# Performance work log

Measured on AMD Instinct MI355X. Metric: run time of the kernel, lower is better.

## Reference

```python
import jax, jax.numpy as jnp
import numpy as np

B, C, N, H = 4, 512, 2048, 8
D = C // H  # per-head depth = 64
EPS = 1e-5


def conv1x1(x, W, b):
    # x: [B, Cin, N], W: [Cout, Cin], b: [Cout]
    return jnp.einsum('oc,bcn->bon', W, x) + b[None, :, None]


def instance_norm(x):
    # normalize over length dim per (batch, channel), no affine
    mu = jnp.mean(x, axis=-1, keepdims=True)
    var = jnp.var(x, axis=-1, keepdims=True)
    return (x - mu) * jax.lax.rsqrt(var + EPS)


def _pipeline(src, tgt, Wq, bq, Wk, bk, Wv, bv, Wm, bm):
    # query from src, key/value from tgt; reshape C -> (D outer, H inner)
    q = conv1x1(src, Wq, bq).reshape(B, D, H, N)
    k = conv1x1(tgt, Wk, bk).reshape(B, D, H, N)
    v = conv1x1(tgt, Wv, bv).reshape(B, D, H, N)
    scores = jnp.einsum('bdhn,bdhm->bhnm', q, k) / jnp.sqrt(jnp.float32(D))
    probs = jax.nn.softmax(scores, axis=-1)
    out = jnp.einsum('bhnm,bdhm->bdhn', probs, v).reshape(B, C, N)
    return conv1x1(out, Wm, bm)


def _mlp(x, W1, b1, W2, b2):
    h = conv1x1(x, W1, b1)
    h = jax.nn.relu(instance_norm(h))
    return conv1x1(h, W2, b2)


def setup_inputs() -> dict:
    key = jax.random.key(0)
    ks = jax.random.split(key, 8)
    s = 0.02
    return {
        'source_features': jax.random.normal(ks[0], (B, C, N), jnp.float32),
        'target_features': jax.random.normal(ks[1], (B, C, N), jnp.float32),
        'Wq': jax.random.normal(ks[2], (C, C), jnp.float32) * s,
        'bq': jnp.zeros((C,), jnp.float32),
        'Wk': jax.random.normal(ks[3], (C, C), jnp.float32) * s,
        'bk': jnp.zeros((C,), jnp.float32),
        'Wv': jax.random.normal(ks[4], (C, C), jnp.float32) * s,
        'bv': jnp.zeros((C,), jnp.float32),
        'Wm': jax.random.normal(ks[5], (C, C), jnp.float32) * s,
        'bm': jnp.zeros((C,), jnp.float32),
        'W1': jax.random.normal(ks[6], (2 * C, 2 * C), jnp.float32) * s,
        'b1': jnp.zeros((2 * C,), jnp.float32),
        'W2': jax.random.normal(ks[7], (C, 2 * C), jnp.float32) * s,
        'b2': jnp.zeros((C,), jnp.float32),
    }


def reference(source_features, target_features, Wq, bq, Wk, bk, Wv, bv, Wm, bm, W1, b1, W2, b2):
    src, tgt = source_features, target_features
    # source update uses ORIGINAL target features
    src_att = _pipeline(src, tgt, Wq, bq, Wk, bk, Wv, bv, Wm, bm)
    src = src + _mlp(jnp.concatenate([src, src_att], axis=1), W1, b1, W2, b2)
    # target update uses the UPDATED source features (in-place semantics of original)
    tgt_att = _pipeline(tgt, src, Wq, bq, Wk, bk, Wv, bv, Wm, bm)
    tgt = tgt + _mlp(jnp.concatenate([tgt, tgt_att], axis=1), W1, b1, W2, b2)
    return src, tgt
```

## Files before the change

### kernel.cpp

```cpp
#include <hip/hip_runtime.h>

#define NN 2048
#define CC 512
#define BB 4
#define HH 8
#define DD 64
#define SCALE 0.18033688011112043f

typedef unsigned short u16;
typedef __attribute__((ext_vector_type(8))) short bf16x8;
typedef __attribute__((ext_vector_type(4))) float f32x4;

extern "C" __device__ float __ocml_native_exp2_f32(float);

__device__ inline u16 f2b(float x) {
    unsigned u = __builtin_bit_cast(unsigned, x);
    u += 0x7fffu + ((u >> 16) & 1u);
    return (u16)(u >> 16);
}
__device__ inline float b2f(u16 h) {
    unsigned u = ((unsigned)h) << 16;
    return __builtin_bit_cast(float, u);
}

#define GLD16(g, l) __builtin_amdgcn_global_load_lds( \
    (const __attribute__((address_space(1))) unsigned int*)(g), \
    (__attribute__((address_space(3))) unsigned int*)(l), 16, 0, 0)

template<int JT>
__device__ __forceinline__ void gemm_core_t(
    const u16* __restrict__ Xa, const u16* __restrict__ Xb, int Ca, int K,
    const u16* __restrict__ Wt, size_t rowBase,
    u16* As, u16* Bs, f32x4 (&acc)[4][JT])
{
    constexpr int OT = JT * 32;
    const int tid = threadIdx.x;
    const int lane = tid & 63, w = tid >> 6;
    const int quad = lane >> 4, l16 = lane & 15;
    const int wrow = w & 1, wcol = w >> 1;
    const int arow = lane >> 2, aseg = lane & 3;

    for (int k0 = 0; k0 < K; k0 += 32) {
        const u16* Xs; int Crow, cc;
        if (k0 < Ca) { Xs = Xa; Crow = Ca; cc = k0; }
        else         { Xs = Xb; Crow = K - Ca; cc = k0 - Ca; }
#pragma unroll
        for (int i = 0; i < 2; ++i) {
            int rl = w * 32 + i * 16 + arow;
            int la = __builtin_amdgcn_readfirstlane((w * 32 + i * 16) * 32);
            GLD16(Xs + (rowBase + rl) * (size_t)Crow + cc + aseg * 8, (char*)As + (size_t)la * 2);
        }
#pragma unroll
        for (int i = 0; i < OT / 64; ++i) {
            int rl = w * (OT / 4) + i * 16 + arow;
            int la = __builtin_amdgcn_readfirstlane((w * (OT / 4) + i * 16) * 32);
            GLD16(Wt + (size_t)rl * K + k0 + aseg * 8, (char*)Bs + (size_t)la * 2);
        }
        __syncthreads();
        bf16x8 av[4], bv[JT];
#pragma unroll
        for (int i = 0; i < 4; ++i)
            av[i] = *(const bf16x8*)&As[(wrow * 64 + i * 16 + l16) * 32 + quad * 8];
#pragma unroll
        for (int jj = 0; jj < JT; ++jj)
            bv[jj] = *(const bf16x8*)&Bs[(wcol * JT * 16 + jj * 16 + l16) * 32 + quad * 8];
#pragma unroll
        for (int i = 0; i < 4; ++i)
#pragma unroll
            for (int jj = 0; jj < JT; ++jj)
                acc[i][jj] = __builtin_amdgcn_mfma_f32_16x16x32_bf16(av[i], bv[jj], acc[i][jj], 0, 0, 0);
        __syncthreads();
    }
}

template<int JT>
__device__ __forceinline__ void gemm_epilogue_t(
    f32x4 (&acc)[4][JT], const float* __restrict__ bias, int mode,
    int b, int n0, int o0, int Cout,
    const float* __restrict__ res, float* __restrict__ outF, u16* __restrict__ outB)
{
    const int tid = threadIdx.x;
    const int lane = tid & 63, w = tid >> 6;
    const int quad = lane >> 4, l16 = lane & 15;
    const int wrow = w & 1, wcol = w >> 1;
    const size_t bN = (size_t)b * NN;
    const int nb0 = n0 + wrow * 64, ob0 = o0 + wcol * JT * 16;

    if (mode == 0) {
#pragma unroll
        for (int j = 0; j < JT; ++j) {
            int o = ob0 + j * 16 + l16;
            float bs = bias[o];
#pragma unroll
            for (int i = 0; i < 4; ++i)
#pragma unroll
                for (int r = 0; r < 4; ++r) {
                    int n = nb0 + i * 16 + quad * 4 + r;
                    outB[(bN + n) * Cout + o] = f2b(acc[i][j][r] + bs);
                }
        }
    } else if (mode == 1) {
#pragma unroll
        for (int j = 0; j < JT; ++j) {
            int o = ob0 + j * 16 + l16;
            float bs = bias[o];
            int h = o >> 6, d = o & 63;
#pragma unroll
            for (int i = 0; i < 4; ++i) {
                int n = nb0 + i * 16 + quad * 4;
                ushort4 pk;
                pk.x = f2b(acc[i][j][0] + bs); pk.y = f2b(acc[i][j][1] + bs);
                pk.z = f2b(acc[i][j][2] + bs); pk.w = f2b(acc[i][j][3] + bs);
                *(ushort4*)&outB[(((size_t)b * HH + h) * DD + d) * NN + n] = pk;
            }
        }
    } else {
#pragma unroll
        for (int j = 0; j < JT; ++j) {
            int o = ob0 + j * 16 + l16;
            float bs = bias[o];
#pragma unroll
            for (int i = 0; i < 4; ++i) {
                int n = nb0 + i * 16 + quad * 4;
                size_t ad = ((size_t)b * Cout + o) * NN + n;
                float4 rv = *(const float4*)&res[ad];
                float4 yv;
                yv.x = acc[i][j][0] + bs + rv.x;
                yv.y = acc[i][j][1] + bs + rv.y;
                yv.z = acc[i][j][2] + bs + rv.z;
                yv.w = acc[i][j][3] + bs + rv.w;
                *(float4*)&outF[ad] = yv;
                if (mode == 2) {
                    outB[(bN + n + 0) * Cout + o] = f2b(yv.x);
                    outB[(bN + n + 1) * Cout + o] = f2b(yv.y);
                    outB[(bN + n + 2) * Cout + o] = f2b(yv.z);
                    outB[(bN + n + 3) * Cout + o] = f2b(yv.w);
                }
            }
        }
    }
}

template<int JT>
__global__ __launch_bounds__(256, (JT == 2 ? 4 : 3)) void gemm_bf16_t(
    const u16* __restrict__ Wb, const float* __restrict__ bias,
    const u16* __restrict__ Xa, const u16* __restrict__ Xb,
    int Ca, int K, int Cout,
    const float* __restrict__ res, float* __restrict__ outF,
    u16* __restrict__ outB, int mode)
{
    __shared__ u16 As[128 * 32];
    __shared__ u16 Bs[JT * 32 * 32];
    const int b = blockIdx.z, n0 = blockIdx.x * 128, o0 = blockIdx.y * (JT * 32);
    f32x4 acc[4][JT] = {};
    gemm_core_t<JT>(Xa, Xb, Ca, K, Wb + (size_t)o0 * K, (size_t)b * NN + n0, As, Bs, acc);
    gemm_epilogue_t<JT>(acc, bias, mode, b, n0, o0, Cout, res, outF, outB);
}

__global__ __launch_bounds__(256, 3) void gemm_qkv(
    const u16* __restrict__ WQ, const float* __restrict__ bQ,
    const u16* __restrict__ XQ, u16* __restrict__ outQ,
    const u16* __restrict__ WK, const float* __restrict__ bK, u16* __restrict__ outK,
    const u16* __restrict__ WV, const float* __restrict__ bV, u16* __restrict__ outV,
    const u16* __restrict__ XKV)
{
    __shared__ u16 As[128 * 32];
    __shared__ u16 Bs[128 * 32];
    const int yb = blockIdx.y;
    const u16* W; const float* bias; const u16* X; u16* outB; int mode, o0;
    if (yb < 4)      { o0 = yb * 128;       W = WQ; bias = bQ; X = XQ;  outB = outQ; mode = 0; }
    else if (yb < 8) { o0 = (yb - 4) * 128; W = WK; bias = bK; X = XKV; outB = outK; mode = 0; }
    else             { o0 = (yb - 8) * 128; W = WV; bias = bV; X = XKV; outB = outV; mode = 1; }
    const int b = blockIdx.z, n0 = blockIdx.x * 128;
    f32x4 acc[4][4] = {};
    gemm_core_t<4>(X, nullptr, 512, 512, W + (size_t)o0 * 512, (size_t)b * NN + n0, As, Bs, acc);
    gemm_epilogue_t<4>(acc, bias, mode, b, n0, o0, 512, nullptr, nullptr, outB);
}

__global__ __launch_bounds__(256, 2) void attn(
    const u16* __restrict__ Qg, const u16* __restrict__ Kg,
    const u16* __restrict__ Vg, u16* __restrict__ Og)
{
    __shared__ __align__(16) u16 Ks[2][64 * 64];
    __shared__ __align__(16) u16 Vt[2][64 * 64];
    __shared__ __align__(16) u16 Ps[128 * 64];
    const int tid = threadIdx.x;
    const int lane = tid & 63, w = tid >> 6;
    const int quad = lane >> 4, l16 = lane & 15;
    const int id = blockIdx.x;
    const int xcd = id & 7, jj = id >> 3;
    const int bh = xcd * 4 + (jj >> 4), nb = jj & 15;
    const int b = bh >> 3, h = bh & 7;
    const int n0 = nb * 128, wn0 = w * 32;
    const int sr0 = w * 16;
    const size_t qkBase = ((size_t)b * NN) * CC + h * DD;
    const size_t vBase  = (((size_t)b * HH + h) * DD) * NN;
    const int r8 = lane >> 3, seg = lane & 7;
    const int segp = seg ^ r8;
    const int lk = l16 & 7;

    const u16* kp0 = Kg + qkBase + (size_t)(sr0 + r8) * CC + segp * 8;
    const u16* kp1 = kp0 + (size_t)8 * CC;
    const u16* vp0 = Vg + vBase + (size_t)(sr0 + r8) * NN + segp * 8;
    const u16* vp1 = vp0 + (size_t)8 * NN;

    bf16x8 qf[2][2];
#pragma unroll
    for (int qs = 0; qs < 2; ++qs) {
        int n = n0 + wn0 + qs * 16 + l16;
#pragma unroll
        for (int ks = 0; ks < 2; ++ks)
            qf[qs][ks] = *(const bf16x8*)&Qg[qkBase + (size_t)n * CC + ks * 32 + quad * 8];
    }

    const short oneb = 0x3F80;
    const bf16x8 ones = {oneb, oneb, oneb, oneb, oneb, oneb, oneb, oneb};
    f32x4 oa[2][4] = {};
    f32x4 lacc[2] = {};

    GLD16(kp0, &Ks[0][sr0 * 64]);
    GLD16(kp1, &Ks[0][(sr0 + 8) * 64]);
    GLD16(vp0, &Vt[0][sr0 * 64]);
    GLD16(vp1, &Vt[0][(sr0 + 8) * 64]);
    kp0 += 64 * CC; kp1 += 64 * CC; vp0 += 64; vp1 += 64;

#define ATTN_PREF(BUF) do { \
        GLD16(kp0, &Ks[BUF][sr0 * 64]); \
        GLD16(kp1, &Ks[BUF][(sr0 + 8) * 64]); \
        GLD16(vp0, &Vt[BUF][sr0 * 64]); \
        GLD16(vp1, &Vt[BUF][(sr0 + 8) * 64]); \
        kp0 += 64 * CC; kp1 += 64 * CC; vp0 += 64; vp1 += 64; \
    } while (0)

#define ATTN_BODY(CUR) do { \
        const u16* ksb = Ks[CUR]; \
        const u16* vtb = Vt[CUR]; \
        f32x4 st[2][4] = {}; \
        _Pragma("unroll") \
        for (int ks = 0; ks < 2; ++ks) { \
            bf16x8 ak[4]; \
            _Pragma("unroll") \
            for (int rt = 0; rt < 4; ++rt) \
                ak[rt] = *(const bf16x8*)&ksb[(rt * 16 + l16) * 64 + ((ks * 4 + quad) ^ lk) * 8]; \
            __builtin_amdgcn_s_setprio(1); \
            _Pragma("unroll") \
            for (int rt = 0; rt < 4; ++rt) \
                _Pragma("unroll") \
                for (int qs = 0; qs < 2; ++qs) \
                    st[qs][rt] = __builtin_amdgcn_mfma_f32_16x16x32_bf16(ak[rt], qf[qs][ks], st[qs][rt], 0, 0, 0); \
            __builtin_amdgcn_s_setprio(0); \
        } \
        _Pragma("unroll") \
        for (int qs = 0; qs < 2; ++qs) { \
            int nrow = wn0 + qs * 16 + l16; \
            _Pragma("unroll") \
            for (int rt = 0; rt < 4; ++rt) { \
                unsigned u0 = __builtin_bit_cast(unsigned, __ocml_native_exp2_f32(st[qs][rt][0])); \
                unsigned u1 = __builtin_bit_cast(unsigned, __ocml_native_exp2_f32(st[qs][rt][1])); \
                unsigned u2 = __builtin_bit_cast(unsigned, __ocml_native_exp2_f32(st[qs][rt][2])); \
                unsigned u3 = __builtin_bit_cast(unsigned, __ocml_native_exp2_f32(st[qs][rt][3])); \
                uint2 t; \
                t.x = __builtin_amdgcn_perm(u1, u0, 0x07060302u); \
                t.y = __builtin_amdgcn_perm(u3, u2, 0x07060302u); \
                int g = (rt * 2 + (quad >> 1)) ^ lk; \
                *(uint2*)&Ps[nrow * 64 + g * 8 + (quad & 1) * 4] = t; \
            } \
        } \
        _Pragma("unroll") \
        for (int ks = 0; ks < 2; ++ks) { \
            bf16x8 pa[2]; \
            _Pragma("unroll") \
            for (int qs = 0; qs < 2; ++qs) \
                pa[qs] = *(const bf16x8*)&Ps[(wn0 + qs * 16 + l16) * 64 + ((ks * 4 + quad) ^ lk) * 8]; \
            bf16x8 vb[4]; \
            _Pragma("unroll") \
            for (int ct = 0; ct < 4; ++ct) \
                vb[ct] = *(const bf16x8*)&vtb[(ct * 16 + l16) * 64 + ((ks * 4 + quad) ^ lk) * 8]; \
            __builtin_amdgcn_s_setprio(1); \
            _Pragma("unroll") \
            for (int ct = 0; ct < 4; ++ct) \
                _Pragma("unroll") \
                for (int qs = 0; qs < 2; ++qs) \
                    oa[qs][ct] = __builtin_amdgcn_mfma_f32_16x16x32_bf16(pa[qs], vb[ct], oa[qs][ct], 0, 0, 0); \
            _Pragma("unroll") \
            for (int qs = 0; qs < 2; ++qs) \
                lacc[qs] = __builtin_amdgcn_mfma_f32_16x16x32_bf16(pa[qs], ones, lacc[qs], 0, 0, 0); \
            __builtin_amdgcn_s_setprio(0); \
        } \
    } while (0)

    for (int it = 0; it < NN / 64; it += 2) {
        __syncthreads();
        ATTN_PREF(1);
        ATTN_BODY(0);
        __syncthreads();
        if (it < NN / 64 - 2)
            ATTN_PREF(0);
        ATTN_BODY(1);
    }
#undef ATTN_PREF
#undef ATTN_BODY

#pragma unroll
    for (int qs = 0; qs < 2; ++qs)
#pragma unroll
        for (int r = 0; r < 4; ++r) {
            float li = 1.f / lacc[qs][r];
            int n = n0 + wn0 + qs * 16 + quad * 4 + r;
#pragma unroll
            for (int ct = 0; ct < 4; ++ct)
                Og[qkBase + (size_t)n * CC + ct * 16 + l16] = f2b(oa[qs][ct][r] * li);
        }
}

__global__ __launch_bounds__(256) void transpose_cvt(
    const float* __restrict__ X, u16* __restrict__ Y)
{
    __shared__ float T[64][65];
    const int tid = threadIdx.x;
    const int n0 = blockIdx.x * 64, c0 = blockIdx.y * 64, b = blockIdx.z;
    const int rr = tid >> 4, cc4 = tid & 15;
#pragma unroll
    for (int p = 0; p < 4; ++p) {
        int cl = p * 16 + rr;
        float4 v = *(const float4*)&X[((size_t)b * CC + c0 + cl) * NN + n0 + cc4 * 4];
        T[cl][cc4 * 4 + 0] = v.x; T[cl][cc4 * 4 + 1] = v.y;
        T[cl][cc4 * 4 + 2] = v.z; T[cl][cc4 * 4 + 3] = v.w;
    }
    __syncthreads();
#pragma unroll
    for (int p = 0; p < 4; ++p) {
        int nl = p * 16 + rr;
        ushort4 pk;
        pk.x = f2b(T[cc4 * 4 + 0][nl]);
        pk.y = f2b(T[cc4 * 4 + 1][nl]);
        pk.z = f2b(T[cc4 * 4 + 2][nl]);
        pk.w = f2b(T[cc4 * 4 + 3][nl]);
        *(ushort4*)&Y[((size_t)b * NN + n0 + nl) * CC + c0 + cc4 * 4] = pk;
    }
}

__global__ __launch_bounds__(256) void prep_weights(
    const float* __restrict__ Wq, const float* __restrict__ Wk,
    const float* __restrict__ Wv, const float* __restrict__ Wm,
    const float* __restrict__ W1, const float* __restrict__ W2,
    u16* oQ, u16* oK, u16* oV, u16* oM, u16* o1, u16* o2)
{
    const float* W; u16* o; int rows, cols, perm; float sc = 1.f;
    switch (blockIdx.z) {
        case 0: W = Wq; o = oQ; rows = 512;  cols = 512;  perm = 1; sc = SCALE; break;
        case 1: W = Wk; o = oK; rows = 512;  cols = 512;  perm = 1; break;
        case 2: W = Wv; o = oV; rows = 512;  cols = 512;  perm = 1; break;
        case 3: W = Wm; o = oM; rows = 512;  cols = 512;  perm = 2; break;
        case 4: W = W1; o = o1; rows = 1024; cols = 1024; perm = 0; break;
        default: W = W2; o = o2; rows = 512; cols = 1024; perm = 0; break;
    }
    int c = blockIdx.x * 256 + threadIdx.x;
    int r = blockIdx.y;
    if (r >= rows || c >= cols) return;
    int sr = r, scol = c;
    if (perm == 1) sr = (r & 63) * 8 + (r >> 6);
    else if (perm == 2) scol = (c & 63) * 8 + (c >> 6);
    o[(size_t)r * cols + c] = f2b(W[(size_t)sr * cols + scol] * sc);
}

__global__ void prep_bias(const float* __restrict__ bq, const float* __restrict__ bk,
                          const float* __restrict__ bv,
                          float* oq, float* ok, float* ov)
{
    int i = blockIdx.x * 256 + threadIdx.x;
    int y = blockIdx.y;
    const float* s = (y == 0) ? bq : (y == 1) ? bk : bv;
    float* o = (y == 0) ? oq : (y == 1) ? ok : ov;
    float v = s[(i & 63) * 8 + (i >> 6)];
    if (y == 0) v *= SCALE;
    o[i] = v;
}

__global__ __launch_bounds__(256) void inorm_p1(
    const u16* __restrict__ X, float* __restrict__ Ssum, float* __restrict__ Ssq)
{
    __shared__ float rs[4][64], rq[4][64];
    const int tid = threadIdx.x;
    const int cl = tid & 63, g = tid >> 6;
    const int c = blockIdx.x * 64 + cl;
    const int b = blockIdx.y, nz = blockIdx.z;
    float s = 0.f, q = 0.f;
    size_t base = ((size_t)b * NN + nz * 256 + g * 64) * 1024 + c;
#pragma unroll 4
    for (int i = 0; i < 64; ++i) {
        float x = b2f(X[base + (size_t)i * 1024]);
        s += x; q += x * x;
    }
    rs[g][cl] = s; rq[g][cl] = q;
    __syncthreads();
    if (g == 0) {
        s = rs[0][cl] + rs[1][cl] + rs[2][cl] + rs[3][cl];
        q = rq[0][cl] + rq[1][cl] + rq[2][cl] + rq[3][cl];
        atomicAdd(&Ssum[b * 1024 + c], s);
        atomicAdd(&Ssq[b * 1024 + c], q);
    }
}

__global__ __launch_bounds__(256) void inorm_p2(
    u16* __restrict__ X, const float* __restrict__ Ssum, const float* __restrict__ Ssq)
{
    const int tid = threadIdx.x;
    const int cl = tid & 63, g = tid >> 6;
    const int c = blockIdx.x * 64 + cl;
    const int b = blockIdx.y, nz = blockIdx.z;
    float mean = Ssum[b * 1024 + c] * (1.f / NN);
    float var  = Ssq[b * 1024 + c] * (1.f / NN) - mean * mean;
    float rstd = rsqrtf(fmaxf(var, 0.f) + 1e-5f);
    size_t base = ((size_t)b * NN + nz * 256 + g * 64) * 1024 + c;
#pragma unroll 4
    for (int i = 0; i < 64; ++i) {
        float x = b2f(X[base + (size_t)i * 1024]);
        x = (x - mean) * rstd;
        X[base + (size_t)i * 1024] = f2b(fmaxf(x, 0.f));
    }
}

extern "C" void kernel_launch(void* const* d_in, const int* in_sizes, int n_in,
                              void* d_out, int out_size, void* d_ws, size_t ws_size,
                              hipStream_t stream)
{
    (void)in_sizes; (void)n_in; (void)out_size; (void)ws_size;
    const float* src = (const float*)d_in[0];
    const float* tgt = (const float*)d_in[1];
    const float* Wq = (const float*)d_in[2];  const float* bq = (const float*)d_in[3];
    const float* Wk = (const float*)d_in[4];  const float* bk = (const float*)d_in[5];
    const float* Wv = (const float*)d_in[6];  const float* bv = (const float*)d_in[7];
    const float* Wm = (const float*)d_in[8];  const float* bm = (const float*)d_in[9];
    const float* W1 = (const float*)d_in[10]; const float* b1 = (const float*)d_in[11];
    const float* W2 = (const float*)d_in[12]; const float* b2 = (const float*)d_in[13];

    char* w = (char*)d_ws;
    u16* WQp = (u16*)(w);
    u16* WKp = (u16*)(w + (512u << 10));
    u16* WVp = (u16*)(w + (1u << 20));
    u16* WMp = (u16*)(w + (3u << 19));
    u16* W1b = (u16*)(w + (2u << 20));
    u16* W2b = (u16*)(w + (4u << 20));
    float* BQp = (float*)(w + (5u << 20));
    float* BKp = BQp + 512;
    float* BVp = BQp + 1024;
    float* STS = BQp + 1536;
    float* STQ = STS + 4096;
    u16* X0 = (u16*)(w + ( 6u << 20));
    u16* X1 = (u16*)(w + (14u << 20));
    u16* B0 = (u16*)(w + (22u << 20));
    u16* B1 = (u16*)(w + (30u << 20));
    u16* B2 = (u16*)(w + (38u << 20));
    u16* B3 = (u16*)(w + (46u << 20));

    float* out = (float*)d_out;
    const size_t R = (size_t)BB * CC * NN;
    dim3 blk(256);

    prep_weights<<<dim3(4, 1024, 6), blk, 0, stream>>>(Wq, Wk, Wv, Wm, W1, W2,
                                                       WQp, WKp, WVp, WMp, W1b, W2b);
    prep_bias<<<dim3(2, 3), blk, 0, stream>>>(bq, bk, bv, BQp, BKp, BVp);
    transpose_cvt<<<dim3(32, 8, 4), blk, 0, stream>>>(src, X0);
    transpose_cvt<<<dim3(32, 8, 4), blk, 0, stream>>>(tgt, X1);

    dim3 gQKV(16, 12, 4), gM(16, 8, 4), gW1(16, 8, 4), gW2(16, 8, 4);

    gemm_qkv<<<gQKV, blk, 0, stream>>>(WQp, BQp, X0, B0, WKp, BKp, B1, WVp, BVp, B2, X1);
    attn<<<dim3(512), blk, 0, stream>>>(B0, B1, B2, B3);
    gemm_bf16_t<2><<<gM, blk, 0, stream>>>(WMp, bm, B3, nullptr, 512, 512, 512, nullptr, nullptr, B0, 0);
    gemm_bf16_t<4><<<gW1, blk, 0, stream>>>(W1b, b1, X0, B0, 512, 1024, 1024, nullptr, nullptr, B1, 0);
    hipMemsetAsync(STS, 0, 8192 * sizeof(float), stream);
    inorm_p1<<<dim3(16, 4, 8), blk, 0, stream>>>(B1, STS, STQ);
    inorm_p2<<<dim3(16, 4, 8), blk, 0, stream>>>(B1, STS, STQ);
    gemm_bf16_t<2><<<gW2, blk, 0, stream>>>(W2b, b2, B1, nullptr, 1024, 1024, 512, src, out, B3, 2);

    gemm_qkv<<<gQKV, blk, 0, stream>>>(WQp, BQp, X1, X0, WKp, BKp, B0, WVp, BVp, B1, B3);
    attn<<<dim3(512), blk, 0, stream>>>(X0, B0, B1, B2);
    gemm_bf16_t<2><<<gM, blk, 0, stream>>>(WMp, bm, B2, nullptr, 512, 512, 512, nullptr, nullptr, X0, 0);
    gemm_bf16_t<4><<<gW1, blk, 0, stream>>>(W1b, b1, X1, X0, 512, 1024, 1024, nullptr, nullptr, B0, 0);
    hipMemsetAsync(STS, 0, 8192 * sizeof(float), stream);
    inorm_p1<<<dim3(16, 4, 8), blk, 0, stream>>>(B0, STS, STQ);
    inorm_p2<<<dim3(16, 4, 8), blk, 0, stream>>>(B0, STS, STQ);
    gemm_bf16_t<2><<<gW2, blk, 0, stream>>>(W2b, b2, B0, nullptr, 1024, 1024, 512, tgt, out + R, nullptr, 3);
}
```

Before: 417.2 us.

## Split attention key tiles across two wave groups and deepen GEMM K-step to 64

The attention kernel now runs 512 threads per block: two groups of four waves each handle half of every 64-key tile (each group computes scores for 32 keys and does the PV product for its half). The partial outputs and row sums are reduced through shared memory at the end. The shared GEMM core loads 64-wide K slices with an XOR-swizzled LDS layout, so it does two MFMA sub-steps per barrier pair instead of one. The aim is more waves in flight for attention and half as many barriers in the GEMMs, at the cost of double the LDS per GEMM block, which may lower occupancy, and an extra cross-group reduction in attention.

```diff
diff --git a/kernel.cpp b/kernel.cpp
--- a/kernel.cpp
+++ b/kernel.cpp
@@ -38,37 +38,43 @@
     const int lane = tid & 63, w = tid >> 6;
     const int quad = lane >> 4, l16 = lane & 15;
     const int wrow = w & 1, wcol = w >> 1;
-    const int arow = lane >> 2, aseg = lane & 3;
-
-    for (int k0 = 0; k0 < K; k0 += 32) {
+    const int arow = lane >> 3, aseg = lane & 7;
+    const int asw = aseg ^ arow;
+    const int lk = l16 & 7;
+
+    for (int k0 = 0; k0 < K; k0 += 64) {
         const u16* Xs; int Crow, cc;
         if (k0 < Ca) { Xs = Xa; Crow = Ca; cc = k0; }
         else         { Xs = Xb; Crow = K - Ca; cc = k0 - Ca; }
 #pragma unroll
-        for (int i = 0; i < 2; ++i) {
-            int rl = w * 32 + i * 16 + arow;
-            int la = __builtin_amdgcn_readfirstlane((w * 32 + i * 16) * 32);
-            GLD16(Xs + (rowBase + rl) * (size_t)Crow + cc + aseg * 8, (char*)As + (size_t)la * 2);
+        for (int i = 0; i < 4; ++i) {
+            int rl = w * 32 + i * 8 + arow;
+            int la = __builtin_amdgcn_readfirstlane((w * 32 + i * 8) * 64);
+            GLD16(Xs + (rowBase + rl) * (size_t)Crow + cc + asw * 8, (char*)As + (size_t)la * 2);
         }
 #pragma unroll
-        for (int i = 0; i < OT / 64; ++i) {
-            int rl = w * (OT / 4) + i * 16 + arow;
-            int la = __builtin_amdgcn_readfirstlane((w * (OT / 4) + i * 16) * 32);
-            GLD16(Wt + (size_t)rl * K + k0 + aseg * 8, (char*)Bs + (size_t)la * 2);
+        for (int i = 0; i < OT / 32; ++i) {
+            int rl = w * (OT / 4) + i * 8 + arow;
+            int la = __builtin_amdgcn_readfirstlane((w * (OT / 4) + i * 8) * 64);
+            GLD16(Wt + (size_t)rl * K + k0 + asw * 8, (char*)Bs + (size_t)la * 2);
         }
         __syncthreads();
-        bf16x8 av[4], bv[JT];
-#pragma unroll
-        for (int i = 0; i < 4; ++i)
-            av[i] = *(const bf16x8*)&As[(wrow * 64 + i * 16 + l16) * 32 + quad * 8];
-#pragma unroll
-        for (int jj = 0; jj < JT; ++jj)
-            bv[jj] = *(const bf16x8*)&Bs[(wcol * JT * 16 + jj * 16 + l16) * 32 + quad * 8];
-#pragma unroll
-        for (int i = 0; i < 4; ++i)
+#pragma unroll
+        for (int kk = 0; kk < 2; ++kk) {
+            const int g = ((kk * 4 + quad) ^ lk) * 8;
+            bf16x8 av[4], bv[JT];
+#pragma unroll
+            for (int i = 0; i < 4; ++i)
+                av[i] = *(const bf16x8*)&As[(wrow * 64 + i * 16 + l16) * 64 + g];
 #pragma unroll
             for (int jj = 0; jj < JT; ++jj)
-                acc[i][jj] = __builtin_amdgcn_mfma_f32_16x16x32_bf16(av[i], bv[jj], acc[i][jj], 0, 0, 0);
+                bv[jj] = *(const bf16x8*)&Bs[(wcol * JT * 16 + jj * 16 + l16) * 64 + g];
+#pragma unroll
+            for (int i = 0; i < 4; ++i)
+#pragma unroll
+                for (int jj = 0; jj < JT; ++jj)
+                    acc[i][jj] = __builtin_amdgcn_mfma_f32_16x16x32_bf16(av[i], bv[jj], acc[i][jj], 0, 0, 0);
+        }
         __syncthreads();
     }
 }
@@ -149,8 +155,8 @@
     const float* __restrict__ res, float* __restrict__ outF,
     u16* __restrict__ outB, int mode)
 {
-    __shared__ u16 As[128 * 32];
-    __shared__ u16 Bs[JT * 32 * 32];
+    __shared__ u16 As[128 * 64];
+    __shared__ u16 Bs[JT * 32 * 64];
     const int b = blockIdx.z, n0 = blockIdx.x * 128, o0 = blockIdx.y * (JT * 32);
     f32x4 acc[4][JT] = {};
     gemm_core_t<JT>(Xa, Xb, Ca, K, Wb + (size_t)o0 * K, (size_t)b * NN + n0, As, Bs, acc);
@@ -164,8 +170,8 @@
     const u16* __restrict__ WV, const float* __restrict__ bV, u16* __restrict__ outV,
     const u16* __restrict__ XKV)
 {
-    __shared__ u16 As[128 * 32];
-    __shared__ u16 Bs[128 * 32];
+    __shared__ u16 As[128 * 64];
+    __shared__ u16 Bs[128 * 64];
     const int yb = blockIdx.y;
     const u16* W; const float* bias; const u16* X; u16* outB; int mode, o0;
     if (yb < 4)      { o0 = yb * 128;       W = WQ; bias = bQ; X = XQ;  outB = outQ; mode = 0; }
@@ -177,32 +183,32 @@
     gemm_epilogue_t<4>(acc, bias, mode, b, n0, o0, 512, nullptr, nullptr, outB);
 }
 
-__global__ __launch_bounds__(256, 2) void attn(
+__global__ __launch_bounds__(512, 4) void attn(
     const u16* __restrict__ Qg, const u16* __restrict__ Kg,
     const u16* __restrict__ Vg, u16* __restrict__ Og)
 {
-    __shared__ __align__(16) u16 Ks[2][64 * 64];
-    __shared__ __align__(16) u16 Vt[2][64 * 64];
-    __shared__ __align__(16) u16 Ps[128 * 64];
+    __shared__ __align__(16) u16 pool[6 * 4096];
+    u16* const Ksb[2] = { pool, pool + 4096 };
+    u16* const Vtb[2] = { pool + 2 * 4096, pool + 3 * 4096 };
+    u16* const Ps = pool + 4 * 4096;
     const int tid = threadIdx.x;
     const int lane = tid & 63, w = tid >> 6;
+    const int qg = w & 3, hv = w >> 2;
     const int quad = lane >> 4, l16 = lane & 15;
     const int id = blockIdx.x;
     const int xcd = id & 7, jj = id >> 3;
     const int bh = xcd * 4 + (jj >> 4), nb = jj & 15;
     const int b = bh >> 3, h = bh & 7;
-    const int n0 = nb * 128, wn0 = w * 32;
-    const int sr0 = w * 16;
+    const int n0 = nb * 128, wn0 = qg * 32;
+    const int sr0 = w * 8;
     const size_t qkBase = ((size_t)b * NN) * CC + h * DD;
     const size_t vBase  = (((size_t)b * HH + h) * DD) * NN;
     const int r8 = lane >> 3, seg = lane & 7;
     const int segp = seg ^ r8;
     const int lk = l16 & 7;
 
-    const u16* kp0 = Kg + qkBase + (size_t)(sr0 + r8) * CC + segp * 8;
-    const u16* kp1 = kp0 + (size_t)8 * CC;
-    const u16* vp0 = Vg + vBase + (size_t)(sr0 + r8) * NN + segp * 8;
-    const u16* vp1 = vp0 + (size_t)8 * NN;
+    const u16* kp = Kg + qkBase + (size_t)(sr0 + r8) * CC + segp * 8;
+    const u16* vp = Vg + vBase + (size_t)(sr0 + r8) * NN + segp * 8;
 
     bf16x8 qf[2][2];
 #pragma unroll
@@ -218,64 +224,59 @@
     f32x4 oa[2][4] = {};
     f32x4 lacc[2] = {};
 
-    GLD16(kp0, &Ks[0][sr0 * 64]);
-    GLD16(kp1, &Ks[0][(sr0 + 8) * 64]);
-    GLD16(vp0, &Vt[0][sr0 * 64]);
-    GLD16(vp1, &Vt[0][(sr0 + 8) * 64]);
-    kp0 += 64 * CC; kp1 += 64 * CC; vp0 += 64; vp1 += 64;
+    GLD16(kp, Ksb[0] + sr0 * 64);
+    GLD16(vp, Vtb[0] + sr0 * 64);
+    kp += 64 * CC; vp += 64;
 
 #define ATTN_PREF(BUF) do { \
-        GLD16(kp0, &Ks[BUF][sr0 * 64]); \
-        GLD16(kp1, &Ks[BUF][(sr0 + 8) * 64]); \
-        GLD16(vp0, &Vt[BUF][sr0 * 64]); \
-        GLD16(vp1, &Vt[BUF][(sr0 + 8) * 64]); \
-        kp0 += 64 * CC; kp1 += 64 * CC; vp0 += 64; vp1 += 64; \
+        GLD16(kp, Ksb[BUF] + sr0 * 64); \
+        GLD16(vp, Vtb[BUF] + sr0 * 64); \
+        kp += 64 * CC; vp += 64; \
     } while (0)
 
 #define ATTN_BODY(CUR) do { \
-        const u16* ksb = Ks[CUR]; \
-        const u16* vtb = Vt[CUR]; \
-        f32x4 st[2][4] = {}; \
+        const u16* ksb = Ksb[CUR]; \
+        const u16* vtb = Vtb[CUR]; \
+        f32x4 st[2][2] = {}; \
         _Pragma("unroll") \
         for (int ks = 0; ks < 2; ++ks) { \
-            bf16x8 ak[4]; \
-            _Pragma("unroll") \
-            for (int rt = 0; rt < 4; ++rt) \
-                ak[rt] = *(const bf16x8*)&ksb[(rt * 16 + l16) * 64 + ((ks * 4 + quad) ^ lk) * 8]; \
+            bf16x8 ak[2]; \
+            _Pragma("unroll") \
+            for (int rtl = 0; rtl < 2; ++rtl) \
+                ak[rtl] = *(const bf16x8*)&ksb[(hv * 32 + rtl * 16 + l16) * 64 + ((ks * 4 + quad) ^ lk) * 8]; \
             __builtin_amdgcn_s_setprio(1); \
             _Pragma("unroll") \
-            for (int rt = 0; rt < 4; ++rt) \
+            for (int rtl = 0; rtl < 2; ++rtl) \
                 _Pragma("unroll") \
                 for (int qs = 0; qs < 2; ++qs) \
-                    st[qs][rt] = __builtin_amdgcn_mfma_f32_16x16x32_bf16(ak[rt], qf[qs][ks], st[qs][rt], 0, 0, 0); \
+                    st[qs][rtl] = __builtin_amdgcn_mfma_f32_16x16x32_bf16(ak[rtl], qf[qs][ks], st[qs][rtl], 0, 0, 0); \
             __builtin_amdgcn_s_setprio(0); \
         } \
         _Pragma("unroll") \
         for (int qs = 0; qs < 2; ++qs) { \
             int nrow = wn0 + qs * 16 + l16; \
             _Pragma("unroll") \
-            for (int rt = 0; rt < 4; ++rt) { \
-                unsigned u0 = __builtin_bit_cast(unsigned, __ocml_native_exp2_f32(st[qs][rt][0])); \
-                unsigned u1 = __builtin_bit_cast(unsigned, __ocml_native_exp2_f32(st[qs][rt][1])); \
-                unsigned u2 = __builtin_bit_cast(unsigned, __ocml_native_exp2_f32(st[qs][rt][2])); \
-                unsigned u3 = __builtin_bit_cast(unsigned, __ocml_native_exp2_f32(st[qs][rt][3])); \
+            for (int rtl = 0; rtl < 2; ++rtl) { \
+                unsigned u0 = __builtin_bit_cast(unsigned, __ocml_native_exp2_f32(st[qs][rtl][0])); \
+                unsigned u1 = __builtin_bit_cast(unsigned, __ocml_native_exp2_f32(st[qs][rtl][1])); \
+                unsigned u2 = __builtin_bit_cast(unsigned, __ocml_native_exp2_f32(st[qs][rtl][2])); \
+                unsigned u3 = __builtin_bit_cast(unsigned, __ocml_native_exp2_f32(st[qs][rtl][3])); \
                 uint2 t; \
                 t.x = __builtin_amdgcn_perm(u1, u0, 0x07060302u); \
                 t.y = __builtin_amdgcn_perm(u3, u2, 0x07060302u); \
-                int g = (rt * 2 + (quad >> 1)) ^ lk; \
+                int g = (((hv * 2 + rtl) * 2 + (quad >> 1))) ^ lk; \
                 *(uint2*)&Ps[nrow * 64 + g * 8 + (quad & 1) * 4] = t; \
             } \
         } \
-        _Pragma("unroll") \
-        for (int ks = 0; ks < 2; ++ks) { \
+        { \
             bf16x8 pa[2]; \
             _Pragma("unroll") \
             for (int qs = 0; qs < 2; ++qs) \
-                pa[qs] = *(const bf16x8*)&Ps[(wn0 + qs * 16 + l16) * 64 + ((ks * 4 + quad) ^ lk) * 8]; \
+                pa[qs] = *(const bf16x8*)&Ps[(wn0 + qs * 16 + l16) * 64 + ((hv * 4 + quad) ^ lk) * 8]; \
             bf16x8 vb[4]; \
             _Pragma("unroll") \
             for (int ct = 0; ct < 4; ++ct) \
-                vb[ct] = *(const bf16x8*)&vtb[(ct * 16 + l16) * 64 + ((ks * 4 + quad) ^ lk) * 8]; \
+                vb[ct] = *(const bf16x8*)&vtb[(ct * 16 + l16) * 64 + ((hv * 4 + quad) ^ lk) * 8]; \
             __builtin_amdgcn_s_setprio(1); \
             _Pragma("unroll") \
             for (int ct = 0; ct < 4; ++ct) \
@@ -301,16 +302,38 @@
 #undef ATTN_PREF
 #undef ATTN_BODY
 
-#pragma unroll
-    for (int qs = 0; qs < 2; ++qs)
-#pragma unroll
-        for (int r = 0; r < 4; ++r) {
-            float li = 1.f / lacc[qs][r];
-            int n = n0 + wn0 + qs * 16 + quad * 4 + r;
+    __syncthreads();
+    float* M = (float*)pool;
+    const int mbase = (qg * 64 + lane) * 40;
+    if (hv == 1) {
+#pragma unroll
+        for (int qs = 0; qs < 2; ++qs)
 #pragma unroll
             for (int ct = 0; ct < 4; ++ct)
-                Og[qkBase + (size_t)n * CC + ct * 16 + l16] = f2b(oa[qs][ct][r] * li);
-        }
+                *(f32x4*)&M[mbase + (qs * 4 + ct) * 4] = oa[qs][ct];
+        *(f32x4*)&M[mbase + 32] = lacc[0];
+        *(f32x4*)&M[mbase + 36] = lacc[1];
+    }
+    __syncthreads();
+    if (hv == 0) {
+#pragma unroll
+        for (int qs = 0; qs < 2; ++qs)
+#pragma unroll
+            for (int ct = 0; ct < 4; ++ct)
+                oa[qs][ct] += *(const f32x4*)&M[mbase + (qs * 4 + ct) * 4];
+        lacc[0] += *(const f32x4*)&M[mbase + 32];
+        lacc[1] += *(const f32x4*)&M[mbase + 36];
+#pragma unroll
+        for (int qs = 0; qs < 2; ++qs)
+#pragma unroll
+            for (int r = 0; r < 4; ++r) {
+                float li = 1.f / lacc[qs][r];
+                int n = n0 + wn0 + qs * 16 + quad * 4 + r;
+#pragma unroll
+                for (int ct = 0; ct < 4; ++ct)
+                    Og[qkBase + (size_t)n * CC + ct * 16 + l16] = f2b(oa[qs][ct][r] * li);
+            }
+    }
 }
 
 __global__ __launch_bounds__(256) void transpose_cvt(
@@ -456,7 +479,7 @@
 
     float* out = (float*)d_out;
     const size_t R = (size_t)BB * CC * NN;
-    dim3 blk(256);
+    dim3 blk(256), blkA(512);
 
     prep_weights<<<dim3(4, 1024, 6), blk, 0, stream>>>(Wq, Wk, Wv, Wm, W1, W2,
                                                        WQp, WKp, WVp, WMp, W1b, W2b);
@@ -467,7 +490,7 @@
     dim3 gQKV(16, 12, 4), gM(16, 8, 4), gW1(16, 8, 4), gW2(16, 8, 4);
 
     gemm_qkv<<<gQKV, blk, 0, stream>>>(WQp, BQp, X0, B0, WKp, BKp, B1, WVp, BVp, B2, X1);
-    attn<<<dim3(512), blk, 0, stream>>>(B0, B1, B2, B3);
+    attn<<<dim3(512), blkA, 0, stream>>>(B0, B1, B2, B3);
     gemm_bf16_t<2><<<gM, blk, 0, stream>>>(WMp, bm, B3, nullptr, 512, 512, 512, nullptr, nullptr, B0, 0);
     gemm_bf16_t<4><<<gW1, blk, 0, stream>>>(W1b, b1, X0, B0, 512, 1024, 1024, nullptr, nullptr, B1, 0);
     hipMemsetAsync(STS, 0, 8192 * sizeof(float), stream);
@@ -476,7 +499,7 @@
     gemm_bf16_t<2><<<gW2, blk, 0, stream>>>(W2b, b2, B1, nullptr, 1024, 1024, 512, src, out, B3, 2);
 
     gemm_qkv<<<gQKV, blk, 0, stream>>>(WQp, BQp, X1, X0, WKp, BKp, B0, WVp, BVp, B1, B3);
-    attn<<<dim3(512), blk, 0, stream>>>(X0, B0, B1, B2);
+    attn<<<dim3(512), blkA, 0, stream>>>(X0, B0, B1, B2);
     gemm_bf16_t<2><<<gM, blk, 0, stream>>>(WMp, bm, B2, nullptr, 512, 512, 512, nullptr, nullptr, X0, 0);
     gemm_bf16_t<4><<<gW1, blk, 0, stream>>>(W1b, b1, X1, X0, 512, 1024, 1024, nullptr, nullptr, B0, 0);
     hipMemsetAsync(STS, 0, 8192 * sizeof(float), stream);
```

Measured after the change: 399.3 us. 1.04x faster.
